# Kernel optimization log

Measured on AMD Instinct MI355X. Metric: run time of the kernel, lower is better.

## Reference

```python
import jax, jax.numpy as jnp
import numpy as np
from math import factorial, sqrt

L_MAX = 3
MUL = 64
# e3nn FullyConnectedTensorProduct instruction order: lexicographic over (l1, l2, l3)
# keeping paths with triangle inequality and matching parity ((-1)^(l1+l2) == (-1)^l3).
PATHS = [(l1, l2, l3)
         for l1 in range(L_MAX + 1)
         for l2 in range(L_MAX + 1)
         for l3 in range(L_MAX + 1)
         if abs(l1 - l2) <= l3 <= l1 + l2 and (l1 + l2 + l3) % 2 == 0]
assert len(PATHS) == 23
N_TO = {l3: sum(1 for p in PATHS if p[2] == l3) for l3 in range(L_MAX + 1)}


def _su2_cg(j1, m1, j2, m2, j3, m3):
    # Complex-basis Clebsch-Gordan coefficient (Racah formula), as in e3nn.
    if m3 != m1 + m2:
        return 0.0
    f = factorial
    vmin = max(-j1 + j2 + m3, -j1 + m1, 0)
    vmax = min(j2 + j3 + m1, j3 - j1 + j2, j3 + m3)
    c = sqrt((2 * j3 + 1) * f(j3 + j1 - j2) * f(j3 - j1 + j2) * f(j1 + j2 - j3)
             * f(j3 + m3) * f(j3 - m3)
             / (f(j1 + j2 + j3 + 1) * f(j1 - m1) * f(j1 + m1) * f(j2 - m2) * f(j2 + m2)))
    s = 0.0
    for v in range(vmin, vmax + 1):
        s += (-1) ** (v + j2 + m2) / f(v) * f(j2 + j3 + m1 - v) * f(j1 - m1 + v) \
             / f(j3 - j1 + j2 - v) / f(j3 + m3 - v) / f(v + j1 - j2 - m3)
    return c * s


def _q(l):
    # Change of basis real -> complex spherical harmonics (e3nn convention).
    q = np.zeros((2 * l + 1, 2 * l + 1), dtype=np.complex128)
    for m in range(-l, 0):
        q[l + m, l + abs(m)] = 1.0 / np.sqrt(2.0)
        q[l + m, l - abs(m)] = -1j / np.sqrt(2.0)
    q[l, l] = 1.0
    for m in range(1, l + 1):
        q[l + m, l + abs(m)] = (-1) ** m / np.sqrt(2.0)
        q[l + m, l - abs(m)] = 1j * (-1) ** m / np.sqrt(2.0)
    return (-1j) ** l * q


def _w3j(l1, l2, l3):
    # Real-basis Wigner 3j tensor, unit Frobenius norm (e3nn's o3.wigner_3j).
    csu2 = np.zeros((2 * l1 + 1, 2 * l2 + 1, 2 * l3 + 1))
    for m1 in range(-l1, l1 + 1):
        for m2 in range(-l2, l2 + 1):
            m3 = m1 + m2
            if -l3 <= m3 <= l3:
                csu2[l1 + m1, l2 + m2, l3 + m3] = _su2_cg(l1, m1, l2, m2, l3, m3)
    q1, q2, q3 = _q(l1), _q(l2), _q(l3)
    c = np.einsum('ij,kl,mn,ikn->jlm', q1, q2, np.conj(q3.T), csu2.astype(np.complex128))
    c = np.real(c)
    return (c / np.linalg.norm(c)).astype(np.float32)


W3J = {p: jnp.asarray(_w3j(*p)) for p in PATHS}
# e3nn 'component' irrep_normalization + 'element' path_normalization:
# per-path coeff = sqrt(ir_out.dim / (n_paths_into_out * mul1 * mul2)).
COEFF = {p: float(np.sqrt((2 * p[2] + 1) / (N_TO[p[2]] * MUL * MUL))) for p in PATHS}


def setup_inputs():
    key = jax.random.key(0)
    kx, kw = jax.random.split(key)
    x = jax.random.normal(kx, (2, 1024, MUL * (L_MAX + 1) ** 2), dtype=jnp.float32)
    weights = jax.random.normal(kw, (len(PATHS), MUL, MUL, MUL), dtype=jnp.float32)
    return {"x": x, "weights": weights}


def reference(x, weights):
    B, N, D = x.shape
    Z = B * N
    xf = x.reshape(Z, D)
    # e3nn layout: blocks of (mul, 2l+1) concatenated over l; offset = MUL * l^2.
    xs = [xf[:, MUL * l * l: MUL * (l + 1) ** 2].reshape(Z, MUL, 2 * l + 1)
          for l in range(L_MAX + 1)]
    acc = [jnp.zeros((Z, MUL, 2 * l + 1), dtype=x.dtype) for l in range(L_MAX + 1)]
    for p, (l1, l2, l3) in enumerate(PATHS):
        c = W3J[(l1, l2, l3)]
        t1 = jnp.einsum('zui,ijk->zujk', xs[l1], c)            # [Z,u,2l2+1,2l3+1]
        t2 = jnp.einsum('zujk,zvj->zuvk', t1, xs[l2])          # [Z,u,v,2l3+1]
        seg = jnp.einsum('zuvk,uvw->zwk', t2, weights[p]) * COEFF[(l1, l2, l3)]
        acc[l3] = acc[l3] + seg
    out = jnp.concatenate([a.reshape(Z, -1) for a in acc], axis=-1)
    return out.reshape(B, N, -1)
```

## Files before the change

kernel.cpp:

```cpp
#include <hip/hip_runtime.h>

struct CD { double re, im; };
constexpr CD cmul(CD a, CD b){ return CD{a.re*b.re - a.im*b.im, a.re*b.im + a.im*b.re}; }
constexpr CD conj_(CD a){ return CD{a.re, -a.im}; }

constexpr double factd(int n){ double r = 1.0; for(int i = 2; i <= n; ++i) r *= (double)i; return r; }
constexpr double csqrt_(double x){
  if (x <= 0.0) return 0.0;
  double g = x > 1.0 ? x : 1.0;
  for (int i = 0; i < 100; ++i) g = 0.5*(g + x/g);
  return g;
}

constexpr double su2_cg(int j1,int m1,int j2,int m2,int j3,int m3){
  if (m3 != m1 + m2) return 0.0;
  int vmin = -j1 + j2 + m3;
  if (-j1 + m1 > vmin) vmin = -j1 + m1;
  if (0 > vmin) vmin = 0;
  int vmax = j2 + j3 + m1;
  if (j3 - j1 + j2 < vmax) vmax = j3 - j1 + j2;
  if (j3 + m3 < vmax) vmax = j3 + m3;
  double c = csqrt_((2.0*j3 + 1.0) * factd(j3 + j1 - j2) * factd(j3 - j1 + j2) * factd(j1 + j2 - j3)
                    * factd(j3 + m3) * factd(j3 - m3)
                    / (factd(j1 + j2 + j3 + 1) * factd(j1 - m1) * factd(j1 + m1)
                       * factd(j2 - m2) * factd(j2 + m2)));
  double s = 0.0;
  for (int v = vmin; v <= vmax; ++v){
    double t = (((v + j2 + m2) & 1) ? -1.0 : 1.0) / factd(v)
               * factd(j2 + j3 + m1 - v) * factd(j1 - m1 + v)
               / factd(j3 - j1 + j2 - v) / factd(j3 + m3 - v) / factd(v + j1 - j2 - m3);
    s += t;
  }
  return c * s;
}

struct QM { CD m[7][7]; };
constexpr QM qmat(int l){
  QM q{};
  double is2 = 1.0 / csqrt_(2.0);
  for (int mm = -l; mm < 0; ++mm){
    q.m[l+mm][l-mm] = CD{is2, 0.0};
    q.m[l+mm][l+mm] = CD{0.0, -is2};
  }
  q.m[l][l] = CD{1.0, 0.0};
  for (int mm = 1; mm <= l; ++mm){
    double sgn = (mm & 1) ? -1.0 : 1.0;
    q.m[l+mm][l+mm] = CD{sgn*is2, 0.0};
    q.m[l+mm][l-mm] = CD{0.0, sgn*is2};
  }
  CD ph = (l % 4 == 0) ? CD{1,0} : (l % 4 == 1) ? CD{0,-1} : (l % 4 == 2) ? CD{-1,0} : CD{0,1};
  for (int r = 0; r < 7; ++r)
    for (int c = 0; c < 7; ++c)
      q.m[r][c] = cmul(ph, q.m[r][c]);
  return q;
}

template<int L1,int L2,int L3> struct W3JT { float v[2*L1+1][2*L2+1][2*L3+1]; };

template<int L1,int L2,int L3>
constexpr W3JT<L1,L2,L3> make_w3j(){
  constexpr int D1 = 2*L1+1, D2 = 2*L2+1, D3 = 2*L3+1;
  QM q1 = qmat(L1), q2 = qmat(L2), q3 = qmat(L3);
  double cg[7][7] = {};
  for (int i = 0; i < D1; ++i)
    for (int k = 0; k < D2; ++k){
      int n = i + k - L1 - L2 + L3;
      if (n >= 0 && n < D3) cg[i][k] = su2_cg(L1, i-L1, L2, k-L2, L3, (i-L1)+(k-L2));
    }
  double c[D1][D2][D3] = {};
  double norm2 = 0.0;
  for (int j = 0; j < D1; ++j)
    for (int l = 0; l < D2; ++l)
      for (int m = 0; m < D3; ++m){
        CD s{0.0, 0.0};
        for (int i = 0; i < D1; ++i)
          for (int k = 0; k < D2; ++k){
            double g = cg[i][k];
            if (g == 0.0) continue;
            int n = i + k - L1 - L2 + L3;
            CD t = cmul(q1.m[i][j], q2.m[k][l]);
            t = cmul(t, conj_(q3.m[n][m]));
            s.re += t.re * g; s.im += t.im * g;
          }
        c[j][l][m] = s.re;
        norm2 += s.re * s.re;
      }
  double inv = 1.0 / csqrt_(norm2);
  W3JT<L1,L2,L3> w{};
  for (int j = 0; j < D1; ++j)
    for (int l = 0; l < D2; ++l)
      for (int m = 0; m < D3; ++m){
        double val = c[j][l][m] * inv;
        if (val < 1e-10 && val > -1e-10) val = 0.0;
        w.v[j][l][m] = (float)val;
      }
  return w;
}

__device__ __constant__ int L3P_[23]  = {0,1,2,3,1,0,2,1,3,2,2,1,3,0,2,1,3,3,2,1,3,0,2};
__device__ __constant__ int SWAPP_[23] = {0,1,1,1,0,0,0,1,1,1,0,0,0,0,0,1,1,0,0,0,0,0,0};
constexpr int K3CUM[24] = {0,1,4,9,16,19,20,25,28,35,40,45,48,55,56,61,64,71,78,83,86,93,94,99};
constexpr size_t PSLICE = 2048ull * 64ull;

typedef __bf16 bf16x8 __attribute__((ext_vector_type(8)));
typedef float  f32x4  __attribute__((ext_vector_type(4)));
typedef float  f32x2  __attribute__((ext_vector_type(2)));

__global__ void pack_w_kernel(const float* __restrict__ w, unsigned short* __restrict__ wp, int total){
  int idx = blockIdx.x * 256 + threadIdx.x;
  if (idx >= total) return;
  int e    = idx & 7;
  int lane = (idx >> 3) & 63;
  int nt   = (idx >> 9) & 3;
  int hf   = (idx >> 11) & 1;
  int s    = (idx >> 12) & 63;
  int p    = idx >> 18;
  int kv = hf*32 + (lane >> 4)*8 + e;
  int wc = nt*16 + (lane & 15);
  int l3 = L3P_[p];
  const float nto[4] = {4.f, 6.f, 7.f, 6.f};
  float coeff = sqrtf((2.f*l3 + 1.f) / (nto[l3] * 4096.f));
  int a = SWAPP_[p] ? kv : s;
  int b = SWAPP_[p] ? s : kv;
  float val = w[(((size_t)p*64 + a)*64 + b)*64 + wc] * coeff;
  unsigned bits = __builtin_bit_cast(unsigned, val);
  unsigned r = (bits + 0x7FFFu + ((bits >> 16) & 1u)) >> 16;
  wp[idx] = (unsigned short)r;
}

__global__ void transpose_x(const float* __restrict__ x, float* __restrict__ xT){
  __shared__ float t[32][33];
  int bx = blockIdx.x, by = blockIdx.y;
  int tx = threadIdx.x & 31, ty = threadIdx.x >> 5;
  #pragma unroll
  for (int r = 0; r < 4; ++r)
    t[ty + r*8][tx] = x[(size_t)(by*32 + ty + r*8)*1024 + bx*32 + tx];
  __syncthreads();
  #pragma unroll
  for (int r = 0; r < 4; ++r)
    xT[(size_t)(bx*32 + ty + r*8)*2048 + by*32 + tx] = t[tx][ty + r*8];
}

template<int P,int L1,int L2,int L3,bool SWAP,int G0,int G,bool PART>
__device__ __forceinline__ void run_slot(
    int tile, const float* __restrict__ xT,
    const unsigned short* __restrict__ wp,
    float* __restrict__ dst, float* lds)
{
  constexpr int K3 = 2*L3+1;
  constexpr int LK = SWAP ? L1 : L2;
  constexpr int LS = SWAP ? L2 : L1;
  constexpr int DK = 2*LK+1, DS = 2*LS+1;
  constexpr auto C = make_w3j<L1,L2,L3>();

  const int lane = threadIdx.x & 63;
  const int wv   = threadIdx.x >> 6;
  const int zc   = tile*16 + (lane & 15);
  float* red = lds;
  float* tl  = lds + 3072 + wv*1040;

  f32x2 xk2[4][DK];
  {
    const float* xkb = xT + (size_t)(64*LK*LK)*2048 + zc;
    const int t0 = wv*32 + (lane >> 4)*8;
    #pragma unroll
    for (int q = 0; q < 4; ++q)
      #pragma unroll
      for (int t = 0; t < DK; ++t){
        float lo = xkb[(size_t)((t0 + 2*q    )*DK + t)*2048];
        float hi = xkb[(size_t)((t0 + 2*q + 1)*DK + t)*2048];
        xk2[q][t] = f32x2{lo, hi};
      }
  }

  const float* xsb = xT + (size_t)(64*LS*LS)*2048 + zc;
  const unsigned short* wu = wp + (size_t)P*262144 + (size_t)wv*2048 + (size_t)lane*8;

  f32x4 acc[G][4];
  #pragma unroll
  for (int a = 0; a < G; ++a)
    #pragma unroll
    for (int b = 0; b < 4; ++b) acc[a][b] = f32x4{0.f,0.f,0.f,0.f};

  auto compute = [&](const bf16x8 (&bf)[4], const float (&xs)[DS]){
    #pragma unroll
    for (int kk = 0; kk < G; ++kk){
      float dk[DK];
      #pragma unroll
      for (int t = 0; t < DK; ++t) dk[t] = 0.f;
      #pragma unroll
      for (int t = 0; t < DK; ++t){
        #pragma unroll
        for (int j = 0; j < DS; ++j){
          const float cv = SWAP ? C.v[t][j][G0+kk] : C.v[j][t][G0+kk];
          if (cv != 0.0f) dk[t] = __builtin_fmaf(xs[j], cv, dk[t]);
        }
      }
      f32x2 af2[4];
      #pragma unroll
      for (int q = 0; q < 4; ++q) af2[q] = f32x2{0.f, 0.f};
      #pragma unroll
      for (int t = 0; t < DK; ++t){
        const f32x2 d2 = f32x2{dk[t], dk[t]};
        #pragma unroll
        for (int q = 0; q < 4; ++q)
          af2[q] += xk2[q][t] * d2;
      }
      bf16x8 af;
      #pragma unroll
      for (int q = 0; q < 4; ++q){
        af[2*q]   = (__bf16)af2[q].x;
        af[2*q+1] = (__bf16)af2[q].y;
      }
      __builtin_amdgcn_s_setprio(1);
      #pragma unroll
      for (int nt = 0; nt < 4; ++nt)
        acc[kk][nt] = __builtin_amdgcn_mfma_f32_16x16x32_bf16(af, bf[nt], acc[kk][nt], 0, 0, 0);
      __builtin_amdgcn_s_setprio(0);
    }
  };

  bf16x8 bA[4], bB[4];
  float xsA[DS], xsB[DS];
  #pragma unroll
  for (int nt = 0; nt < 4; ++nt)
    bA[nt] = *reinterpret_cast<const bf16x8*>(wu + nt*512);
  #pragma unroll
  for (int j = 0; j < DS; ++j) xsA[j] = xsb[(size_t)j*2048];

  for (int s = 0; s < 64; s += 2){
    #pragma unroll
    for (int nt = 0; nt < 4; ++nt)
      bB[nt] = *reinterpret_cast<const bf16x8*>(wu + 4096 + nt*512);
    #pragma unroll
    for (int j = 0; j < DS; ++j) xsB[j] = xsb[(size_t)(DS + j)*2048];

    compute(bA, xsA);

    #pragma unroll
    for (int nt = 0; nt < 4; ++nt)
      bA[nt] = *reinterpret_cast<const bf16x8*>(wu + 8192 + nt*512);
    #pragma unroll
    for (int j = 0; j < DS; ++j) xsA[j] = xsb[(size_t)(2*DS + j)*2048];

    compute(bB, xsB);

    wu  += 8192;
    xsb += (size_t)2*DS*2048;
  }

  constexpr int Gh = (G + 1) / 2;
  static_assert(Gh <= 3, "red[] sized for Gh<=3");
  auto store_kk = [&](int kk, const f32x4 (&sum)[4]){
    if constexpr (PART){
      #pragma unroll
      for (int nt = 0; nt < 4; ++nt)
        #pragma unroll
        for (int r = 0; r < 4; ++r)
          tl[(((lane >> 4)*4 + r))*65 + nt*16 + (lane & 15)] = sum[nt][r];
      #pragma unroll
      for (int zr = 0; zr < 16; ++zr){
        float v = tl[zr*65 + lane];
        dst[(size_t)K3CUM[P]*PSLICE + ((size_t)(tile*16 + zr)*K3 + (G0+kk))*64 + lane] = v;
      }
    } else {
      #pragma unroll
      for (int nt = 0; nt < 4; ++nt)
        #pragma unroll
        for (int r = 0; r < 4; ++r){
          int zl = ((lane >> 4) << 2) + r;
          int wc = nt*16 + (lane & 15);
          unsafeAtomicAdd(dst + (size_t)(tile*16 + zl)*1024 + 64*L3*L3 + wc*K3 + (G0+kk),
                          sum[nt][r]);
        }
    }
  };

  if (wv == 1){
    #pragma unroll
    for (int kk = 0; kk < Gh; ++kk)
      #pragma unroll
      for (int nt = 0; nt < 4; ++nt)
        *reinterpret_cast<f32x4*>(&red[((kk*4 + nt)*64 + lane)*4]) = acc[kk][nt];
  }
  __syncthreads();
  if (wv == 0){
    #pragma unroll
    for (int kk = 0; kk < Gh; ++kk){
      f32x4 sum[4];
      #pragma unroll
      for (int nt = 0; nt < 4; ++nt){
        f32x4 o = *reinterpret_cast<const f32x4*>(&red[((kk*4 + nt)*64 + lane)*4]);
        sum[nt] = acc[kk][nt] + o;
      }
      store_kk(kk, sum);
    }
  }
  if constexpr (G > Gh){
    if (wv == 0){
      #pragma unroll
      for (int kk = Gh; kk < G; ++kk)
        #pragma unroll
        for (int nt = 0; nt < 4; ++nt)
          *reinterpret_cast<f32x4*>(&red[(((kk-Gh)*4 + nt)*64 + lane)*4]) = acc[kk][nt];
    }
    __syncthreads();
    if (wv == 1){
      #pragma unroll
      for (int kk = Gh; kk < G; ++kk){
        f32x4 sum[4];
        #pragma unroll
        for (int nt = 0; nt < 4; ++nt){
          f32x4 o = *reinterpret_cast<const f32x4*>(&red[(((kk-Gh)*4 + nt)*64 + lane)*4]);
          sum[nt] = acc[kk][nt] + o;
        }
        store_kk(kk, sum);
      }
    }
  }
}

template<bool PART>
__global__ __launch_bounds__(128, 3) void tp_main(const float* __restrict__ xT,
    const unsigned short* __restrict__ wp, float* __restrict__ dst)
{
  __shared__ __align__(16) float lds[5152];
  const int slot = blockIdx.x >> 7;
  const int tile = blockIdx.x & 127;
  switch (slot){
    case 0:  run_slot< 6,1,1,2,false,0,5,PART>(tile,xT,wp,dst,lds); break;
    case 1:  run_slot<16,2,3,3,true ,0,3,PART>(tile,xT,wp,dst,lds); break;
    case 2:  run_slot<20,3,2,3,false,0,3,PART>(tile,xT,wp,dst,lds); break;
    case 3:  run_slot<14,2,2,2,false,0,3,PART>(tile,xT,wp,dst,lds); break;
    case 4:  run_slot<15,2,3,1,true ,0,3,PART>(tile,xT,wp,dst,lds); break;
    case 5:  run_slot<19,3,2,1,false,0,3,PART>(tile,xT,wp,dst,lds); break;
    case 6:  run_slot< 8,1,2,3,true ,0,4,PART>(tile,xT,wp,dst,lds); break;
    case 7:  run_slot<12,2,1,3,false,0,4,PART>(tile,xT,wp,dst,lds); break;
    case 8:  run_slot<22,3,3,2,false,0,2,PART>(tile,xT,wp,dst,lds); break;
    case 9:  run_slot<22,3,3,2,false,2,2,PART>(tile,xT,wp,dst,lds); break;
    case 10: run_slot< 9,1,3,2,true ,0,3,PART>(tile,xT,wp,dst,lds); break;
    case 11: run_slot<16,2,3,3,true ,3,2,PART>(tile,xT,wp,dst,lds); break;
    case 12: run_slot<16,2,3,3,true ,5,2,PART>(tile,xT,wp,dst,lds); break;
    case 13: run_slot<20,3,2,3,false,3,2,PART>(tile,xT,wp,dst,lds); break;
    case 14: run_slot<20,3,2,3,false,5,2,PART>(tile,xT,wp,dst,lds); break;
    case 15: run_slot< 2,0,2,2,true ,0,5,PART>(tile,xT,wp,dst,lds); break;
    case 16: run_slot<10,2,0,2,false,0,5,PART>(tile,xT,wp,dst,lds); break;
    case 17: run_slot<11,2,1,1,false,0,3,PART>(tile,xT,wp,dst,lds); break;
    case 18: run_slot< 7,1,2,1,true ,0,3,PART>(tile,xT,wp,dst,lds); break;
    case 19: run_slot<18,3,1,2,false,0,3,PART>(tile,xT,wp,dst,lds); break;
    case 20: run_slot< 8,1,2,3,true ,4,3,PART>(tile,xT,wp,dst,lds); break;
    case 21: run_slot<12,2,1,3,false,4,3,PART>(tile,xT,wp,dst,lds); break;
    case 22: run_slot<14,2,2,2,false,3,2,PART>(tile,xT,wp,dst,lds); break;
    case 23: run_slot< 9,1,3,2,true ,3,2,PART>(tile,xT,wp,dst,lds); break;
    case 24: run_slot<18,3,1,2,false,3,2,PART>(tile,xT,wp,dst,lds); break;
    case 25: run_slot<22,3,3,2,false,4,1,PART>(tile,xT,wp,dst,lds); break;
    case 26: run_slot<21,3,3,0,false,0,1,PART>(tile,xT,wp,dst,lds); break;
    case 27: run_slot< 3,0,3,3,true ,0,4,PART>(tile,xT,wp,dst,lds); break;
    case 28: run_slot<17,3,0,3,false,0,4,PART>(tile,xT,wp,dst,lds); break;
    case 29: run_slot< 3,0,3,3,true ,4,3,PART>(tile,xT,wp,dst,lds); break;
    case 30: run_slot<17,3,0,3,false,4,3,PART>(tile,xT,wp,dst,lds); break;
    case 31: run_slot< 1,0,1,1,true ,0,3,PART>(tile,xT,wp,dst,lds); break;
    case 32: run_slot< 4,1,0,1,false,0,3,PART>(tile,xT,wp,dst,lds); break;
    case 33: run_slot<13,2,2,0,false,0,1,PART>(tile,xT,wp,dst,lds); break;
    case 34: run_slot< 5,1,1,0,false,0,1,PART>(tile,xT,wp,dst,lds); break;
    case 35: run_slot< 0,0,0,0,false,0,1,PART>(tile,xT,wp,dst,lds); break;
    default: break;
  }
}

__global__ void gather_out(const float* __restrict__ part, float* __restrict__ out){
  const int z = blockIdx.x;
  const int t = threadIdx.x;
  const int w = t & 63;
  const int g = t >> 6;
  float* ob = out + (size_t)z*1024;
  auto rd = [&](int p, int K3p, int k){
    return part[(size_t)K3CUM[p]*PSLICE + ((size_t)z*K3p + k)*64 + w];
  };
  if (g == 0){
    ob[w] = rd(0,1,0) + rd(5,1,0) + rd(13,1,0) + rd(21,1,0);
  } else if (g == 1){
    #pragma unroll
    for (int k = 0; k < 3; ++k)
      ob[64 + w*3 + k] = rd(1,3,k) + rd(4,3,k) + rd(7,3,k)
                       + rd(11,3,k) + rd(15,3,k) + rd(19,3,k);
  } else if (g == 2){
    #pragma unroll
    for (int k = 0; k < 5; ++k)
      ob[256 + w*5 + k] = rd(2,5,k) + rd(6,5,k) + rd(9,5,k) + rd(10,5,k)
                        + rd(14,5,k) + rd(18,5,k) + rd(22,5,k);
  } else {
    #pragma unroll
    for (int k = 0; k < 7; ++k)
      ob[576 + w*7 + k] = rd(3,7,k) + rd(8,7,k) + rd(12,7,k)
                        + rd(16,7,k) + rd(17,7,k) + rd(20,7,k);
  }
}

extern "C" void kernel_launch(void* const* d_in, const int* in_sizes, int n_in,
                              void* d_out, int out_size, void* d_ws, size_t ws_size,
                              hipStream_t stream)
{
  const float* x = (const float*)d_in[0];
  const float* w = (const float*)d_in[1];
  float* out = (float*)d_out;

  const size_t packB = 23ull*64*2*4*64*8 * sizeof(unsigned short);
  const size_t xTB   = 1024ull*2048*sizeof(float);
  const size_t partB = 99ull*PSLICE*sizeof(float);
  const size_t slack = 65536;
  const int totalW = 23*64*2*4*64*8;

  unsigned short* wp = (unsigned short*)d_ws;
  float* xT   = (float*)((char*)d_ws + packB);
  float* part = (float*)((char*)d_ws + packB + xTB);

  if (ws_size < packB + xTB + slack) return;

  pack_w_kernel<<<(totalW + 255)/256, 256, 0, stream>>>(w, wp, totalW);
  dim3 tg(32, 64);
  transpose_x<<<tg, 256, 0, stream>>>(x, xT);

  if (ws_size >= packB + xTB + partB + slack){
    tp_main<true><<<36*128, 128, 0, stream>>>(xT, wp, part);
    gather_out<<<2048, 256, 0, stream>>>(part, out);
  } else {
    hipMemsetAsync(d_out, 0, (size_t)out_size * sizeof(float), stream);
    tp_main<false><<<36*128, 128, 0, stream>>>(xT, wp, out);
  }
}
```

Measured before the change: 214.7 us.

## Split path work into finer slots for better load balance; stop unrolling main loop

```diff
diff --git a/kernel.cpp b/kernel.cpp
--- a/kernel.cpp
+++ b/kernel.cpp
@@ -173,7 +173,7 @@
       }
   }
 
-  const float* xsb = xT + (size_t)(64*LS*LS)*2048 + zc;
+  const float* xsp = xT + (size_t)(64*LS*LS)*2048 + zc;
   const unsigned short* wu = wp + (size_t)P*262144 + (size_t)wv*2048 + (size_t)lane*8;
 
   f32x4 acc[G][4];
@@ -221,32 +221,33 @@
   };
 
   bf16x8 bA[4], bB[4];
-  float xsA[DS], xsB[DS];
+  float xs[DS], xn[DS];
   #pragma unroll
   for (int nt = 0; nt < 4; ++nt)
     bA[nt] = *reinterpret_cast<const bf16x8*>(wu + nt*512);
   #pragma unroll
-  for (int j = 0; j < DS; ++j) xsA[j] = xsb[(size_t)j*2048];
-
+  for (int j = 0; j < DS; ++j) xs[j] = xsp[(size_t)j*2048];
+
+  #pragma unroll 1
   for (int s = 0; s < 64; s += 2){
     #pragma unroll
     for (int nt = 0; nt < 4; ++nt)
       bB[nt] = *reinterpret_cast<const bf16x8*>(wu + 4096 + nt*512);
     #pragma unroll
-    for (int j = 0; j < DS; ++j) xsB[j] = xsb[(size_t)(DS + j)*2048];
-
-    compute(bA, xsA);
+    for (int j = 0; j < DS; ++j) xn[j] = xsp[(size_t)(DS + j)*2048];
+
+    compute(bA, xs);
 
     #pragma unroll
     for (int nt = 0; nt < 4; ++nt)
       bA[nt] = *reinterpret_cast<const bf16x8*>(wu + 8192 + nt*512);
     #pragma unroll
-    for (int j = 0; j < DS; ++j) xsA[j] = xsb[(size_t)(2*DS + j)*2048];
-
-    compute(bB, xsB);
+    for (int j = 0; j < DS; ++j) xs[j] = xsp[(size_t)(2*DS + j)*2048];
+
+    compute(bB, xn);
 
     wu  += 8192;
-    xsb += (size_t)2*DS*2048;
+    xsp += (size_t)2*DS*2048;
   }
 
   constexpr int Gh = (G + 1) / 2;
@@ -328,42 +329,56 @@
   const int slot = blockIdx.x >> 7;
   const int tile = blockIdx.x & 127;
   switch (slot){
-    case 0:  run_slot< 6,1,1,2,false,0,5,PART>(tile,xT,wp,dst,lds); break;
-    case 1:  run_slot<16,2,3,3,true ,0,3,PART>(tile,xT,wp,dst,lds); break;
-    case 2:  run_slot<20,3,2,3,false,0,3,PART>(tile,xT,wp,dst,lds); break;
-    case 3:  run_slot<14,2,2,2,false,0,3,PART>(tile,xT,wp,dst,lds); break;
-    case 4:  run_slot<15,2,3,1,true ,0,3,PART>(tile,xT,wp,dst,lds); break;
-    case 5:  run_slot<19,3,2,1,false,0,3,PART>(tile,xT,wp,dst,lds); break;
-    case 6:  run_slot< 8,1,2,3,true ,0,4,PART>(tile,xT,wp,dst,lds); break;
-    case 7:  run_slot<12,2,1,3,false,0,4,PART>(tile,xT,wp,dst,lds); break;
-    case 8:  run_slot<22,3,3,2,false,0,2,PART>(tile,xT,wp,dst,lds); break;
-    case 9:  run_slot<22,3,3,2,false,2,2,PART>(tile,xT,wp,dst,lds); break;
-    case 10: run_slot< 9,1,3,2,true ,0,3,PART>(tile,xT,wp,dst,lds); break;
-    case 11: run_slot<16,2,3,3,true ,3,2,PART>(tile,xT,wp,dst,lds); break;
-    case 12: run_slot<16,2,3,3,true ,5,2,PART>(tile,xT,wp,dst,lds); break;
-    case 13: run_slot<20,3,2,3,false,3,2,PART>(tile,xT,wp,dst,lds); break;
-    case 14: run_slot<20,3,2,3,false,5,2,PART>(tile,xT,wp,dst,lds); break;
-    case 15: run_slot< 2,0,2,2,true ,0,5,PART>(tile,xT,wp,dst,lds); break;
-    case 16: run_slot<10,2,0,2,false,0,5,PART>(tile,xT,wp,dst,lds); break;
-    case 17: run_slot<11,2,1,1,false,0,3,PART>(tile,xT,wp,dst,lds); break;
-    case 18: run_slot< 7,1,2,1,true ,0,3,PART>(tile,xT,wp,dst,lds); break;
-    case 19: run_slot<18,3,1,2,false,0,3,PART>(tile,xT,wp,dst,lds); break;
-    case 20: run_slot< 8,1,2,3,true ,4,3,PART>(tile,xT,wp,dst,lds); break;
-    case 21: run_slot<12,2,1,3,false,4,3,PART>(tile,xT,wp,dst,lds); break;
-    case 22: run_slot<14,2,2,2,false,3,2,PART>(tile,xT,wp,dst,lds); break;
-    case 23: run_slot< 9,1,3,2,true ,3,2,PART>(tile,xT,wp,dst,lds); break;
-    case 24: run_slot<18,3,1,2,false,3,2,PART>(tile,xT,wp,dst,lds); break;
-    case 25: run_slot<22,3,3,2,false,4,1,PART>(tile,xT,wp,dst,lds); break;
-    case 26: run_slot<21,3,3,0,false,0,1,PART>(tile,xT,wp,dst,lds); break;
-    case 27: run_slot< 3,0,3,3,true ,0,4,PART>(tile,xT,wp,dst,lds); break;
-    case 28: run_slot<17,3,0,3,false,0,4,PART>(tile,xT,wp,dst,lds); break;
-    case 29: run_slot< 3,0,3,3,true ,4,3,PART>(tile,xT,wp,dst,lds); break;
-    case 30: run_slot<17,3,0,3,false,4,3,PART>(tile,xT,wp,dst,lds); break;
-    case 31: run_slot< 1,0,1,1,true ,0,3,PART>(tile,xT,wp,dst,lds); break;
-    case 32: run_slot< 4,1,0,1,false,0,3,PART>(tile,xT,wp,dst,lds); break;
-    case 33: run_slot<13,2,2,0,false,0,1,PART>(tile,xT,wp,dst,lds); break;
-    case 34: run_slot< 5,1,1,0,false,0,1,PART>(tile,xT,wp,dst,lds); break;
-    case 35: run_slot< 0,0,0,0,false,0,1,PART>(tile,xT,wp,dst,lds); break;
+    case 0:  run_slot<16,2,3,3,true ,0,2,PART>(tile,xT,wp,dst,lds); break;
+    case 1:  run_slot<16,2,3,3,true ,2,2,PART>(tile,xT,wp,dst,lds); break;
+    case 2:  run_slot<16,2,3,3,true ,4,2,PART>(tile,xT,wp,dst,lds); break;
+    case 3:  run_slot<16,2,3,3,true ,6,1,PART>(tile,xT,wp,dst,lds); break;
+    case 4:  run_slot<20,3,2,3,false,0,2,PART>(tile,xT,wp,dst,lds); break;
+    case 5:  run_slot<20,3,2,3,false,2,2,PART>(tile,xT,wp,dst,lds); break;
+    case 6:  run_slot<20,3,2,3,false,4,2,PART>(tile,xT,wp,dst,lds); break;
+    case 7:  run_slot<20,3,2,3,false,6,1,PART>(tile,xT,wp,dst,lds); break;
+    case 8:  run_slot<22,3,3,2,false,0,1,PART>(tile,xT,wp,dst,lds); break;
+    case 9:  run_slot<22,3,3,2,false,1,1,PART>(tile,xT,wp,dst,lds); break;
+    case 10: run_slot<22,3,3,2,false,2,1,PART>(tile,xT,wp,dst,lds); break;
+    case 11: run_slot<22,3,3,2,false,3,1,PART>(tile,xT,wp,dst,lds); break;
+    case 12: run_slot<22,3,3,2,false,4,1,PART>(tile,xT,wp,dst,lds); break;
+    case 13: run_slot<14,2,2,2,false,0,2,PART>(tile,xT,wp,dst,lds); break;
+    case 14: run_slot<14,2,2,2,false,2,2,PART>(tile,xT,wp,dst,lds); break;
+    case 15: run_slot<14,2,2,2,false,4,1,PART>(tile,xT,wp,dst,lds); break;
+    case 16: run_slot< 8,1,2,3,true ,0,3,PART>(tile,xT,wp,dst,lds); break;
+    case 17: run_slot< 8,1,2,3,true ,3,3,PART>(tile,xT,wp,dst,lds); break;
+    case 18: run_slot< 8,1,2,3,true ,6,1,PART>(tile,xT,wp,dst,lds); break;
+    case 19: run_slot<12,2,1,3,false,0,3,PART>(tile,xT,wp,dst,lds); break;
+    case 20: run_slot<12,2,1,3,false,3,3,PART>(tile,xT,wp,dst,lds); break;
+    case 21: run_slot<12,2,1,3,false,6,1,PART>(tile,xT,wp,dst,lds); break;
+    case 22: run_slot<15,2,3,1,true ,0,2,PART>(tile,xT,wp,dst,lds); break;
+    case 23: run_slot<15,2,3,1,true ,2,1,PART>(tile,xT,wp,dst,lds); break;
+    case 24: run_slot<19,3,2,1,false,0,2,PART>(tile,xT,wp,dst,lds); break;
+    case 25: run_slot<19,3,2,1,false,2,1,PART>(tile,xT,wp,dst,lds); break;
+    case 26: run_slot< 6,1,1,2,false,0,3,PART>(tile,xT,wp,dst,lds); break;
+    case 27: run_slot< 6,1,1,2,false,3,2,PART>(tile,xT,wp,dst,lds); break;
+    case 28: run_slot< 9,1,3,2,true ,0,3,PART>(tile,xT,wp,dst,lds); break;
+    case 29: run_slot< 9,1,3,2,true ,3,2,PART>(tile,xT,wp,dst,lds); break;
+    case 30: run_slot<18,3,1,2,false,0,3,PART>(tile,xT,wp,dst,lds); break;
+    case 31: run_slot<18,3,1,2,false,3,2,PART>(tile,xT,wp,dst,lds); break;
+    case 32: run_slot< 7,1,2,1,true ,0,3,PART>(tile,xT,wp,dst,lds); break;
+    case 33: run_slot<11,2,1,1,false,0,3,PART>(tile,xT,wp,dst,lds); break;
+    case 34: run_slot<21,3,3,0,false,0,1,PART>(tile,xT,wp,dst,lds); break;
+    case 35: run_slot<13,2,2,0,false,0,1,PART>(tile,xT,wp,dst,lds); break;
+    case 36: run_slot< 3,0,3,3,true ,0,3,PART>(tile,xT,wp,dst,lds); break;
+    case 37: run_slot< 3,0,3,3,true ,3,3,PART>(tile,xT,wp,dst,lds); break;
+    case 38: run_slot< 3,0,3,3,true ,6,1,PART>(tile,xT,wp,dst,lds); break;
+    case 39: run_slot<17,3,0,3,false,0,3,PART>(tile,xT,wp,dst,lds); break;
+    case 40: run_slot<17,3,0,3,false,3,3,PART>(tile,xT,wp,dst,lds); break;
+    case 41: run_slot<17,3,0,3,false,6,1,PART>(tile,xT,wp,dst,lds); break;
+    case 42: run_slot< 2,0,2,2,true ,0,3,PART>(tile,xT,wp,dst,lds); break;
+    case 43: run_slot< 2,0,2,2,true ,3,2,PART>(tile,xT,wp,dst,lds); break;
+    case 44: run_slot<10,2,0,2,false,0,3,PART>(tile,xT,wp,dst,lds); break;
+    case 45: run_slot<10,2,0,2,false,3,2,PART>(tile,xT,wp,dst,lds); break;
+    case 46: run_slot< 1,0,1,1,true ,0,3,PART>(tile,xT,wp,dst,lds); break;
+    case 47: run_slot< 4,1,0,1,false,0,3,PART>(tile,xT,wp,dst,lds); break;
+    case 48: run_slot< 5,1,1,0,false,0,1,PART>(tile,xT,wp,dst,lds); break;
+    case 49: run_slot< 0,0,0,0,false,0,1,PART>(tile,xT,wp,dst,lds); break;
     default: break;
   }
 }
@@ -408,7 +423,7 @@
   const size_t packB = 23ull*64*2*4*64*8 * sizeof(unsigned short);
   const size_t xTB   = 1024ull*2048*sizeof(float);
   const size_t partB = 99ull*PSLICE*sizeof(float);
-  const size_t slack = 65536;
+  const size_t slack = 131072;
   const int totalW = 23*64*2*4*64*8;
 
   unsigned short* wp = (unsigned short*)d_ws;
@@ -422,10 +437,10 @@
   transpose_x<<<tg, 256, 0, stream>>>(x, xT);
 
   if (ws_size >= packB + xTB + partB + slack){
-    tp_main<true><<<36*128, 128, 0, stream>>>(xT, wp, part);
+    tp_main<true><<<50*128, 128, 0, stream>>>(xT, wp, part);
     gather_out<<<2048, 256, 0, stream>>>(part, out);
   } else {
     hipMemsetAsync(d_out, 0, (size_t)out_size * sizeof(float), stream);
-    tp_main<false><<<36*128, 128, 0, stream>>>(xT, wp, out);
-  }
-}
+    tp_main<false><<<50*128, 128, 0, stream>>>(xT, wp, out);
+  }
+}
```

New measurement: 212.0 us. About the same (-1.3%).
